# Kernel tuning notes

Measured on AMD Instinct MI355X. Metric: run time of the kernel, lower is better.

## Reference

```python
import jax, jax.numpy as jnp
import numpy as np

N = 50000
E = 800000
F_IN = 256
HID = 64
HEADS = 4
CLASSES = 8
NEG_SLOPE = 0.2  # PyG GATConv default


def setup_inputs() -> dict:
    key = jax.random.key(0)
    ks = jax.random.split(key, 10)
    x = jax.random.normal(ks[0], (N, F_IN), jnp.float32)
    edge_index = jax.random.randint(ks[1], (2, E), 0, N, dtype=jnp.int32)
    # layer 1: feature -> hidden, heads=4, concat
    W1 = jax.random.normal(ks[2], (F_IN, HEADS * HID), jnp.float32) / np.sqrt(F_IN).astype(np.float32)
    att1_src = jax.random.normal(ks[3], (HEADS, HID), jnp.float32) / np.sqrt(HID).astype(np.float32)
    att1_dst = jax.random.normal(ks[4], (HEADS, HID), jnp.float32) / np.sqrt(HID).astype(np.float32)
    b1 = jnp.zeros((HEADS * HID,), jnp.float32)
    # layer 2: hidden*heads -> classes, heads=1
    W2 = jax.random.normal(ks[5], (HEADS * HID, CLASSES), jnp.float32) / np.sqrt(HEADS * HID).astype(np.float32)
    att2_src = jax.random.normal(ks[6], (1, CLASSES), jnp.float32) / np.sqrt(CLASSES).astype(np.float32)
    att2_dst = jax.random.normal(ks[7], (1, CLASSES), jnp.float32) / np.sqrt(CLASSES).astype(np.float32)
    b2 = jnp.zeros((CLASSES,), jnp.float32)
    return {"x": x, "edge_index": edge_index, "W1": W1, "att1_src": att1_src,
            "att1_dst": att1_dst, "b1": b1, "W2": W2, "att2_src": att2_src,
            "att2_dst": att2_dst, "b2": b2}


def _gat_conv(x, W, a_src, a_dst, b, src, dst, heads, ch, n):
    # h: [N, H, C] per-head projected features
    h = (x @ W).reshape(n, heads, ch)
    alpha_src = jnp.einsum('nhc,hc->nh', h, a_src)  # [N, H]
    alpha_dst = jnp.einsum('nhc,hc->nh', h, a_dst)  # [N, H]
    # per-edge attention logits (gather along edges)
    e = jax.nn.leaky_relu(alpha_src[src] + alpha_dst[dst], NEG_SLOPE)  # [E, H]
    # segment softmax over edges sharing a destination node
    e_max = jax.ops.segment_max(e, dst, num_segments=n)  # [N, H]
    ex = jnp.exp(e - e_max[dst])
    denom = jax.ops.segment_sum(ex, dst, num_segments=n)  # [N, H]
    alpha = ex / denom[dst]  # self-loops guarantee denom > 0
    # weighted scatter-sum of source messages
    out = jax.ops.segment_sum(alpha[..., None] * h[src], dst, num_segments=n)  # [N, H, C]
    return out.reshape(n, heads * ch) + b


def reference(x, edge_index, W1, att1_src, att1_dst, b1, W2, att2_src, att2_dst, b2):
    n = x.shape[0]
    # PyG GATConv adds self-loops by default
    loop = jnp.arange(n, dtype=edge_index.dtype)
    src = jnp.concatenate([edge_index[0], loop])
    dst = jnp.concatenate([edge_index[1], loop])
    h = _gat_conv(x, W1, att1_src, att1_dst, b1, src, dst, HEADS, HID, n)
    h = jax.nn.relu(h)
    # dropout is identity in eval mode (training=self.training)
    out = _gat_conv(h, W2, att2_src, att2_dst, b2, src, dst, 1, CLASSES, n)
    return jax.nn.log_softmax(out, axis=1)
```

## Files before the change

kernel.cpp:

```cpp
#include <hip/hip_runtime.h>
#include <math.h>

#define NNODES 50000
#define NEDGES 800000
#define ETOT   850000
#define SLOPE  0.2f
#define BSLOTS 96
#define CPAD   16
#define NTILE  782
#define BBLK   518

typedef unsigned short ushort_t;
typedef unsigned int   uint_t;
typedef __attribute__((ext_vector_type(8))) __bf16 bf16x8;
typedef __attribute__((ext_vector_type(4))) float  floatx4;

__device__ __forceinline__ float leaky(float v) { return fmaxf(v, SLOPE * v); }

__device__ __forceinline__ ushort_t f2bf(float f) {
    uint_t u = __float_as_uint(f);
    uint_t r = (u + 0x7fffu + ((u >> 16) & 1u)) >> 16;
    return (ushort_t)r;
}
__device__ __forceinline__ float lof(uint_t u) { return __uint_as_float(u << 16); }
__device__ __forceinline__ float hif(uint_t u) { return __uint_as_float(u & 0xffff0000u); }

__device__ __forceinline__ float hsel(float4 v, int h) {
    float t0 = (h & 1) ? v.y : v.x;
    float t1 = (h & 1) ? v.w : v.z;
    return (h & 2) ? t1 : t0;
}

__device__ __forceinline__ int esrc(const int* ei, int e) { return e < NEDGES ? ei[e]          : e - NEDGES; }
__device__ __forceinline__ int edst(const int* ei, int e) { return e < NEDGES ? ei[NEDGES + e] : e - NEDGES; }

__global__ void prep_k(const float* __restrict__ W1, ushort_t* __restrict__ W1c,
                       const float* __restrict__ b1, const float* __restrict__ W2,
                       float* __restrict__ b1p, float* __restrict__ W2p,
                       int* __restrict__ cnt) {
    int bid = blockIdx.x, tid = threadIdx.x;
    int gtid = bid * 256 + tid;
    if (bid < 256) {
        int k = gtid >> 8, n = gtid & 255;
        W1c[(k >> 5) * 8192 + n * 32 + (k & 31)] = f2bf(W1[gtid]);
    } else if (bid == 256) {
        int chp = tid;
        int q = chp & 63, cc = q >> 2, t = q & 3;
        int ch = (chp & 192) | (t * 16 + cc);
        b1p[chp] = b1[ch];
        #pragma unroll
        for (int j = 0; j < 8; ++j) W2p[chp * 8 + j] = W2[ch * 8 + j];
    }
    for (int i = gtid; i < NNODES * CPAD; i += 257 * 256) cnt[i] = 0;
}

__global__ __launch_bounds__(256) void gb_k(const float* __restrict__ X,
                                            const ushort_t* __restrict__ W1c,
                                            const float* __restrict__ att_s,
                                            const float* __restrict__ att_d,
                                            ushort_t* __restrict__ h1b,
                                            float* __restrict__ as1,
                                            float* __restrict__ ad1,
                                            const int* __restrict__ ei,
                                            int* __restrict__ cnt,
                                            int* __restrict__ bkt) {
    __shared__ ushort_t Als[64 * 40];
    __shared__ ushort_t Bls[256 * 40];
    int tid = threadIdx.x;

    if (blockIdx.x >= NTILE) {
        for (int e = (blockIdx.x - NTILE) * 256 + tid; e < ETOT; e += BBLK * 256) {
            int d = edst(ei, e), s = esrc(ei, e);
            int pos = atomicAdd(&cnt[d * CPAD], 1);
            if (pos < BSLOTS) bkt[d * BSLOTS + pos] = s;
        }
        return;
    }

    int row0 = blockIdx.x * 64;
    int wv = tid >> 6, lane = tid & 63, c15 = lane & 15, quad = lane >> 4;
    floatx4 acc[4][4] = {};

    for (int kc = 0; kc < 8; ++kc) {
        __syncthreads();
        {
            int r = tid >> 3, c4 = tid & 7;
            #pragma unroll
            for (int p = 0; p < 2; ++p) {
                int rr = r + p * 32;
                int row = row0 + rr;
                float4 v = make_float4(0.f, 0.f, 0.f, 0.f);
                if (row < NNODES) v = *(const float4*)&X[(size_t)row * 256 + kc * 32 + c4 * 4];
                uint2 pk;
                pk.x = (uint_t)f2bf(v.x) | ((uint_t)f2bf(v.y) << 16);
                pk.y = (uint_t)f2bf(v.z) | ((uint_t)f2bf(v.w) << 16);
                *(uint2*)&Als[rr * 40 + c4 * 4] = pk;
            }
        }
        {
            const uint4* srcp = (const uint4*)(W1c + kc * 8192);
            #pragma unroll
            for (int c = 0; c < 4; ++c) {
                int el = tid + c * 256;
                uint4 v = srcp[el];
                int n = el >> 2, kk8 = (el & 3) * 8;
                *(uint4*)&Bls[n * 40 + kk8] = v;
            }
        }
        __syncthreads();
        uint4 af[4], bfr[4];
        #pragma unroll
        for (int t = 0; t < 4; ++t)
            af[t] = *(const uint4*)&Als[(t * 16 + c15) * 40 + quad * 8];
        #pragma unroll
        for (int t = 0; t < 4; ++t)
            bfr[t] = *(const uint4*)&Bls[(wv * 64 + t * 16 + c15) * 40 + quad * 8];
        #pragma unroll
        for (int tm = 0; tm < 4; ++tm)
            #pragma unroll
            for (int tn = 0; tn < 4; ++tn)
                acc[tm][tn] = __builtin_amdgcn_mfma_f32_16x16x32_bf16(
                    __builtin_bit_cast(bf16x8, af[tm]),
                    __builtin_bit_cast(bf16x8, bfr[tn]),
                    acc[tm][tn], 0, 0, 0);
    }

    float asv[4], adv[4];
    #pragma unroll
    for (int tn = 0; tn < 4; ++tn) {
        asv[tn] = att_s[wv * 64 + tn * 16 + c15];
        adv[tn] = att_d[wv * 64 + tn * 16 + c15];
    }
    float ps[4][4], pd[4][4];
    #pragma unroll
    for (int tm = 0; tm < 4; ++tm)
        #pragma unroll
        for (int r = 0; r < 4; ++r) {
            float vs = 0.f, vd = 0.f;
            #pragma unroll
            for (int tn = 0; tn < 4; ++tn) {
                float a = acc[tm][tn][r];
                vs += a * asv[tn]; vd += a * adv[tn];
            }
            ps[tm][r] = vs; pd[tm][r] = vd;
        }
    #pragma unroll
    for (int tm = 0; tm < 4; ++tm) {
        #pragma unroll
        for (int r = 0; r < 4; ++r) {
            int row = row0 + tm * 16 + quad * 4 + r;
            if (row < NNODES) {
                uint2 pk;
                pk.x = (uint_t)f2bf(acc[tm][0][r]) | ((uint_t)f2bf(acc[tm][1][r]) << 16);
                pk.y = (uint_t)f2bf(acc[tm][2][r]) | ((uint_t)f2bf(acc[tm][3][r]) << 16);
                *(uint2*)&h1b[(size_t)row * 256 + wv * 64 + c15 * 4] = pk;
            }
        }
    }
    #pragma unroll
    for (int off = 1; off < 16; off <<= 1)
        #pragma unroll
        for (int tm = 0; tm < 4; ++tm)
            #pragma unroll
            for (int r = 0; r < 4; ++r) {
                ps[tm][r] += __shfl_xor(ps[tm][r], off, 64);
                pd[tm][r] += __shfl_xor(pd[tm][r], off, 64);
            }
    if (c15 == 0) {
        #pragma unroll
        for (int tm = 0; tm < 4; ++tm)
            #pragma unroll
            for (int r = 0; r < 4; ++r) {
                int row = row0 + tm * 16 + quad * 4 + r;
                if (row < NNODES) {
                    as1[row * 4 + wv] = ps[tm][r];
                    ad1[row * 4 + wv] = pd[tm][r];
                }
            }
    }
}

__global__ __launch_bounds__(256) void f1_k(const int* __restrict__ cnt,
                                            const int* __restrict__ bkt,
                                            const float* __restrict__ as1,
                                            const float* __restrict__ ad1,
                                            const ushort_t* __restrict__ h1b,
                                            const float* __restrict__ b1p,
                                            const float* __restrict__ W2p,
                                            const float* __restrict__ a2sw,
                                            const float* __restrict__ a2dw,
                                            float* __restrict__ h2,
                                            float* __restrict__ a2s,
                                            float* __restrict__ a2d) {
    int wv = threadIdx.x >> 6;
    int lane = threadIdx.x & 63;
    int half = lane >> 5, l32 = lane & 31;
    int node = blockIdx.x * 8 + wv * 2 + half;
    int h = l32 >> 3;
    int deg = min(cnt[node * CPAD], BSLOTS);
    const int* bp = bkt + (size_t)node * BSLOTS;
    float4 advec = *(const float4*)&ad1[(size_t)node * 4];
    __shared__ float wls[4][2][32][4];

    float acc[8] = {};
    float dn0, dn1, dn2, dn3;
    if (deg <= 32) {
        bool act = l32 < deg;
        int s_reg = node;
        if (act) s_reg = bp[l32];
        float4 av = *(const float4*)&as1[(size_t)s_reg * 4];
        float e0 = act ? __expf(leaky(av.x + advec.x)) : 0.f;
        float e1 = act ? __expf(leaky(av.y + advec.y)) : 0.f;
        float e2 = act ? __expf(leaky(av.z + advec.z)) : 0.f;
        float e3 = act ? __expf(leaky(av.w + advec.w)) : 0.f;
        *(float4*)&wls[wv][half][l32][0] = make_float4(e0, e1, e2, e3);
        dn0 = e0; dn1 = e1; dn2 = e2; dn3 = e3;
        #pragma unroll
        for (int off = 16; off; off >>= 1) {
            dn0 += __shfl_xor(dn0, off, 64);
            dn1 += __shfl_xor(dn1, off, 64);
            dn2 += __shfl_xor(dn2, off, 64);
            dn3 += __shfl_xor(dn3, off, 64);
        }
        int nb = (deg + 7) & ~7;
        int sbase = half << 5;
        for (int base = 0; base < nb; base += 8) {
            #pragma unroll
            for (int u = 0; u < 8; ++u) {
                int e = base + u;
                int se = __shfl(s_reg, sbase + e, 64);
                float w = wls[wv][half][e][h];
                uint4 v = *(const uint4*)&h1b[(size_t)se * 256 + l32 * 8];
                acc[0] += w * lof(v.x); acc[1] += w * hif(v.x);
                acc[2] += w * lof(v.y); acc[3] += w * hif(v.y);
                acc[4] += w * lof(v.z); acc[5] += w * hif(v.z);
                acc[6] += w * lof(v.w); acc[7] += w * hif(v.w);
            }
        }
    } else {
        dn0 = dn1 = dn2 = dn3 = 0.f;
        for (int j = l32; j < deg; j += 32) {
            int s = bp[j];
            float4 av = *(const float4*)&as1[(size_t)s * 4];
            dn0 += __expf(leaky(av.x + advec.x));
            dn1 += __expf(leaky(av.y + advec.y));
            dn2 += __expf(leaky(av.z + advec.z));
            dn3 += __expf(leaky(av.w + advec.w));
        }
        #pragma unroll
        for (int off = 16; off; off >>= 1) {
            dn0 += __shfl_xor(dn0, off, 64);
            dn1 += __shfl_xor(dn1, off, 64);
            dn2 += __shfl_xor(dn2, off, 64);
            dn3 += __shfl_xor(dn3, off, 64);
        }
        float advh = hsel(advec, h);
        int cmax = deg - 1;
        for (int base = 0; base < deg; base += 8) {
            #pragma unroll
            for (int u = 0; u < 8; ++u) {
                int e = base + u;
                int ce = min(e, cmax);
                int se = bp[ce];
                float ash = as1[(size_t)se * 4 + h];
                float w = (e < deg) ? __expf(leaky(ash + advh)) : 0.f;
                uint4 v = *(const uint4*)&h1b[(size_t)se * 256 + l32 * 8];
                acc[0] += w * lof(v.x); acc[1] += w * hif(v.x);
                acc[2] += w * lof(v.y); acc[3] += w * hif(v.y);
                acc[4] += w * lof(v.z); acc[5] += w * hif(v.z);
                acc[6] += w * lof(v.w); acc[7] += w * hif(v.w);
            }
        }
    }
    float rdh = 1.f / hsel(make_float4(dn0, dn1, dn2, dn3), h);
    #pragma unroll
    for (int c = 0; c < 8; ++c) acc[c] *= rdh;

    int k0 = l32 * 8;
    float4 ba = *(const float4*)&b1p[k0];
    float4 bb = *(const float4*)&b1p[k0 + 4];
    float xv[8];
    xv[0] = fmaxf(acc[0] + ba.x, 0.f); xv[1] = fmaxf(acc[1] + ba.y, 0.f);
    xv[2] = fmaxf(acc[2] + ba.z, 0.f); xv[3] = fmaxf(acc[3] + ba.w, 0.f);
    xv[4] = fmaxf(acc[4] + bb.x, 0.f); xv[5] = fmaxf(acc[5] + bb.y, 0.f);
    xv[6] = fmaxf(acc[6] + bb.z, 0.f); xv[7] = fmaxf(acc[7] + bb.w, 0.f);
    float p[8] = {};
    #pragma unroll
    for (int q = 0; q < 8; ++q) {
        const float4* w2p = (const float4*)&W2p[(size_t)(k0 + q) * 8];
        float4 wa = w2p[0], wb = w2p[1];
        p[0] += xv[q] * wa.x; p[1] += xv[q] * wa.y; p[2] += xv[q] * wa.z; p[3] += xv[q] * wa.w;
        p[4] += xv[q] * wb.x; p[5] += xv[q] * wb.y; p[6] += xv[q] * wb.z; p[7] += xv[q] * wb.w;
    }
    #pragma unroll
    for (int off = 16; off; off >>= 1)
        #pragma unroll
        for (int c = 0; c < 8; ++c) p[c] += __shfl_xor(p[c], off, 64);
    if (l32 == 0) {
        *(float4*)&h2[(size_t)node * 8]     = make_float4(p[0], p[1], p[2], p[3]);
        *(float4*)&h2[(size_t)node * 8 + 4] = make_float4(p[4], p[5], p[6], p[7]);
        float vs = 0.f, vd = 0.f;
        #pragma unroll
        for (int c = 0; c < 8; ++c) { vs += p[c] * a2sw[c]; vd += p[c] * a2dw[c]; }
        a2s[node] = vs; a2d[node] = vd;
    }
}

__global__ __launch_bounds__(256) void f2_k(const int* __restrict__ cnt,
                                            const int* __restrict__ bkt,
                                            const float* __restrict__ a2s,
                                            const float* __restrict__ a2d,
                                            const float* __restrict__ h2,
                                            const float* __restrict__ b2,
                                            float* __restrict__ out) {
    int wv = threadIdx.x >> 6;
    int lane = threadIdx.x & 63;
    int half = lane >> 5, l32 = lane & 31;
    int node = blockIdx.x * 8 + wv * 2 + half;
    int deg = min(cnt[node * CPAD], BSLOTS);
    const int* bp = bkt + (size_t)node * BSLOTS;
    float adv = a2d[node];

    float acc_a = 0.f, acc_b = 0.f;
    float den;
    int c = l32 & 7, eg = l32 >> 3;
    if (deg <= 32) {
        bool act = l32 < deg;
        int s_reg = node;
        if (act) s_reg = bp[l32];
        float ex = act ? __expf(leaky(a2s[s_reg] + adv)) : 0.f;
        den = ex;
        #pragma unroll
        for (int off = 16; off; off >>= 1) den += __shfl_xor(den, off, 64);
        int nb = (deg + 7) & ~7;
        int sbase = half << 5;
        for (int base = 0; base < nb; base += 8) {
            int e1 = base + eg, e2 = base + 4 + eg;
            int se1 = __shfl(s_reg, sbase + e1, 64);
            float w1 = __shfl(ex,    sbase + e1, 64);
            int se2 = __shfl(s_reg, sbase + e2, 64);
            float w2 = __shfl(ex,    sbase + e2, 64);
            acc_a += w1 * h2[(size_t)se1 * 8 + c];
            acc_b += w2 * h2[(size_t)se2 * 8 + c];
        }
    } else {
        den = 0.f;
        for (int j = l32; j < deg; j += 32) {
            int s = bp[j];
            den += __expf(leaky(a2s[s] + adv));
        }
        #pragma unroll
        for (int off = 16; off; off >>= 1) den += __shfl_xor(den, off, 64);
        int cmax = deg - 1;
        for (int base = 0; base < deg; base += 4) {
            int e = base + eg, ce = min(e, cmax);
            int se = bp[ce];
            float w = (e < deg) ? __expf(leaky(a2s[se] + adv)) : 0.f;
            acc_a += w * h2[(size_t)se * 8 + c];
        }
    }
    float acc = acc_a + acc_b;
    acc += __shfl_xor(acc, 8, 64);
    acc += __shfl_xor(acc, 16, 64);
    acc /= den;

    float v = acc + b2[c];
    float mx = v;
    #pragma unroll
    for (int off = 1; off < 8; off <<= 1) mx = fmaxf(mx, __shfl_xor(mx, off, 64));
    float ex2 = __expf(v - mx);
    float ss = ex2;
    #pragma unroll
    for (int off = 1; off < 8; off <<= 1) ss += __shfl_xor(ss, off, 64);
    if (l32 < 8) out[(size_t)node * 8 + c] = v - (mx + __logf(ss));
}

extern "C" void kernel_launch(void* const* d_in, const int* in_sizes, int n_in,
                              void* d_out, int out_size, void* d_ws, size_t ws_size,
                              hipStream_t stream) {
    const float* x    = (const float*)d_in[0];
    const int*   ei   = (const int*)  d_in[1];
    const float* W1   = (const float*)d_in[2];
    const float* a1sw = (const float*)d_in[3];
    const float* a1dw = (const float*)d_in[4];
    const float* b1   = (const float*)d_in[5];
    const float* W2   = (const float*)d_in[6];
    const float* a2sw = (const float*)d_in[7];
    const float* a2dw = (const float*)d_in[8];
    const float* b2   = (const float*)d_in[9];
    float* out = (float*)d_out;

    ushort_t* h1b = (ushort_t*)d_ws;
    ushort_t* W1c = h1b + 12800000;
    float* as1  = (float*)(W1c + 65536);
    float* ad1  = as1 + 200000;
    float* h2   = ad1 + 200000;
    float* a2s  = h2  + 400000;
    float* a2d  = a2s + 50000;
    float* b1p  = a2d + 50000;
    float* W2p  = b1p + 256;
    int*   cnt  = (int*)(W2p + 2048);
    int*   bkt  = cnt + NNODES * CPAD;

    prep_k<<<257, 256, 0, stream>>>(W1, W1c, b1, W2, b1p, W2p, cnt);

    gb_k<<<NTILE + BBLK, 256, 0, stream>>>(x, W1c, a1sw, a1dw, h1b, as1, ad1,
                                           ei, cnt, bkt);

    f1_k<<<NNODES / 8, 256, 0, stream>>>(cnt, bkt, as1, ad1, h1b, b1p, W2p,
                                         a2sw, a2dw, h2, a2s, a2d);

    f2_k<<<NNODES / 8, 256, 0, stream>>>(cnt, bkt, a2s, a2d, h2, b2, out);
}
```

Before: 288.1 us.

## Process two nodes per half-wave in f1 with register-prefetched neighbor gathers

The layer-1 aggregation kernel now gives each half-wave two destination nodes instead of one. It issues the gathers of the first 16 bf16 neighbor rows for both nodes into registers before computing the softmax weights. It then alternates consuming one batch while prefetching the next, to keep more independent memory requests in flight and hide gather latency. The grid is halved to match. The cost is much higher register pressure, which can lower occupancy, and a wave now takes the slow path whenever any of its four nodes has more than 32 neighbors.

```diff
diff --git a/kernel.cpp b/kernel.cpp
--- a/kernel.cpp
+++ b/kernel.cpp
@@ -177,6 +177,109 @@
                     ad1[row * 4 + wv] = pd[tm][r];
                 }
             }
+    }
+}
+
+
+#define PREL(SREG, BASE, VV)                                                    \
+    {                                                                           \
+        _Pragma("unroll")                                                       \
+        for (int u = 0; u < 8; ++u) {                                           \
+            int se = __shfl(SREG, sbase + (BASE) + u, 64);                      \
+            VV[u] = *(const uint4*)&h1b[(size_t)se * 256 + l32 * 8];            \
+        }                                                                       \
+    }
+#define CONS(CH, BASE, VV, AC)                                                  \
+    {                                                                           \
+        _Pragma("unroll")                                                       \
+        for (int u = 0; u < 8; ++u) {                                           \
+            float w = wls[wv][half][CH][(BASE) + u][h];                         \
+            uint4 v = VV[u];                                                    \
+            AC[0] += w * lof(v.x); AC[1] += w * hif(v.x);                       \
+            AC[2] += w * lof(v.y); AC[3] += w * hif(v.y);                       \
+            AC[4] += w * lof(v.z); AC[5] += w * hif(v.z);                       \
+            AC[6] += w * lof(v.w); AC[7] += w * hif(v.w);                       \
+        }                                                                       \
+    }
+
+__device__ __forceinline__ float4 slow_chain(int node, int deg, const int* bp,
+                                             float4 advec, int l32, int h,
+                                             const float* __restrict__ as1,
+                                             const ushort_t* __restrict__ h1b,
+                                             float* acc) {
+    float dn0 = 0.f, dn1 = 0.f, dn2 = 0.f, dn3 = 0.f;
+    for (int j = l32; j < deg; j += 32) {
+        int s = bp[j];
+        float4 av = *(const float4*)&as1[(size_t)s * 4];
+        dn0 += __expf(leaky(av.x + advec.x));
+        dn1 += __expf(leaky(av.y + advec.y));
+        dn2 += __expf(leaky(av.z + advec.z));
+        dn3 += __expf(leaky(av.w + advec.w));
+    }
+    #pragma unroll
+    for (int off = 16; off; off >>= 1) {
+        dn0 += __shfl_xor(dn0, off, 64);
+        dn1 += __shfl_xor(dn1, off, 64);
+        dn2 += __shfl_xor(dn2, off, 64);
+        dn3 += __shfl_xor(dn3, off, 64);
+    }
+    float advh = hsel(advec, h);
+    int cmax = deg - 1;
+    for (int base = 0; base < deg; base += 8) {
+        #pragma unroll
+        for (int u = 0; u < 8; ++u) {
+            int e = base + u;
+            int ce = min(e, cmax);
+            int se = bp[ce];
+            float ash = as1[(size_t)se * 4 + h];
+            float w = (e < deg) ? __expf(leaky(ash + advh)) : 0.f;
+            uint4 v = *(const uint4*)&h1b[(size_t)se * 256 + l32 * 8];
+            acc[0] += w * lof(v.x); acc[1] += w * hif(v.x);
+            acc[2] += w * lof(v.y); acc[3] += w * hif(v.y);
+            acc[4] += w * lof(v.z); acc[5] += w * hif(v.z);
+            acc[6] += w * lof(v.w); acc[7] += w * hif(v.w);
+        }
+    }
+    return make_float4(dn0, dn1, dn2, dn3);
+}
+
+__device__ __forceinline__ void epi(float* acc, float rdh, int node, int l32,
+                                    const float* __restrict__ b1p,
+                                    const float* __restrict__ W2p,
+                                    const float* __restrict__ a2sw,
+                                    const float* __restrict__ a2dw,
+                                    float* __restrict__ h2,
+                                    float* __restrict__ a2s,
+                                    float* __restrict__ a2d) {
+    int k0 = l32 * 8;
+    float4 ba = *(const float4*)&b1p[k0];
+    float4 bb = *(const float4*)&b1p[k0 + 4];
+    float xv[8];
+    #pragma unroll
+    for (int c = 0; c < 8; ++c) acc[c] *= rdh;
+    xv[0] = fmaxf(acc[0] + ba.x, 0.f); xv[1] = fmaxf(acc[1] + ba.y, 0.f);
+    xv[2] = fmaxf(acc[2] + ba.z, 0.f); xv[3] = fmaxf(acc[3] + ba.w, 0.f);
+    xv[4] = fmaxf(acc[4] + bb.x, 0.f); xv[5] = fmaxf(acc[5] + bb.y, 0.f);
+    xv[6] = fmaxf(acc[6] + bb.z, 0.f); xv[7] = fmaxf(acc[7] + bb.w, 0.f);
+    float p[8] = {};
+    #pragma unroll
+    for (int q = 0; q < 8; ++q) {
+        const float4* w2p = (const float4*)&W2p[(size_t)(k0 + q) * 8];
+        float4 wa2 = w2p[0], wb2 = w2p[1];
+        p[0] += xv[q] * wa2.x; p[1] += xv[q] * wa2.y; p[2] += xv[q] * wa2.z; p[3] += xv[q] * wa2.w;
+        p[4] += xv[q] * wb2.x; p[5] += xv[q] * wb2.y; p[6] += xv[q] * wb2.z; p[7] += xv[q] * wb2.w;
+    }
+    #pragma unroll
+    for (int off = 16; off; off >>= 1)
+        #pragma unroll
+        for (int c = 0; c < 8; ++c) p[c] += __shfl_xor(p[c], off, 64);
+    if (l32 == 0) {
+        *(float4*)&h2[(size_t)node * 8]     = make_float4(p[0], p[1], p[2], p[3]);
+        *(float4*)&h2[(size_t)node * 8 + 4] = make_float4(p[4], p[5], p[6], p[7]);
+        float vs = 0.f, vd = 0.f;
+        #pragma unroll
+        for (int c = 0; c < 8; ++c) { vs += p[c] * a2sw[c]; vd += p[c] * a2dw[c]; }
+        a2s[node] = vs; a2d[node] = vd;
     }
 }
 
@@ -195,115 +298,83 @@
     int wv = threadIdx.x >> 6;
     int lane = threadIdx.x & 63;
     int half = lane >> 5, l32 = lane & 31;
-    int node = blockIdx.x * 8 + wv * 2 + half;
+    int base = blockIdx.x * 16 + wv * 4;
+    int nodeA = base + half;
+    int nodeB = base + 2 + half;
     int h = l32 >> 3;
-    int deg = min(cnt[node * CPAD], BSLOTS);
-    const int* bp = bkt + (size_t)node * BSLOTS;
-    float4 advec = *(const float4*)&ad1[(size_t)node * 4];
-    __shared__ float wls[4][2][32][4];
-
-    float acc[8] = {};
-    float dn0, dn1, dn2, dn3;
-    if (deg <= 32) {
-        bool act = l32 < deg;
-        int s_reg = node;
-        if (act) s_reg = bp[l32];
-        float4 av = *(const float4*)&as1[(size_t)s_reg * 4];
-        float e0 = act ? __expf(leaky(av.x + advec.x)) : 0.f;
-        float e1 = act ? __expf(leaky(av.y + advec.y)) : 0.f;
-        float e2 = act ? __expf(leaky(av.z + advec.z)) : 0.f;
-        float e3 = act ? __expf(leaky(av.w + advec.w)) : 0.f;
-        *(float4*)&wls[wv][half][l32][0] = make_float4(e0, e1, e2, e3);
-        dn0 = e0; dn1 = e1; dn2 = e2; dn3 = e3;
+    int sbase = half << 5;
+    __shared__ float wls[4][2][2][32][4];
+
+    int degA = min(cnt[nodeA * CPAD], BSLOTS);
+    int degB = min(cnt[nodeB * CPAD], BSLOTS);
+    const int* bpA = bkt + (size_t)nodeA * BSLOTS;
+    const int* bpB = bkt + (size_t)nodeB * BSLOTS;
+    float4 advA = *(const float4*)&ad1[(size_t)nodeA * 4];
+    float4 advB = *(const float4*)&ad1[(size_t)nodeB * 4];
+
+    int dmA = max(degA, __shfl_xor(degA, 32, 64));
+    int dmB = max(degB, __shfl_xor(degB, 32, 64));
+
+    float accA[8] = {}, accB[8] = {};
+    float rdhA, rdhB;
+
+    if (max(dmA, dmB) <= 32) {
+        bool actA = l32 < degA, actB = l32 < degB;
+        int sA = actA ? bpA[l32] : nodeA;
+        int sB = actB ? bpB[l32] : nodeB;
+        float4 avA = *(const float4*)&as1[(size_t)sA * 4];
+        float4 avB = *(const float4*)&as1[(size_t)sB * 4];
+
+        uint4 vaA[8], vbA[8], vaB[8], vbB[8];
+        PREL(sA, 0, vaA); PREL(sB, 0, vaB);
+        PREL(sA, 8, vbA); PREL(sB, 8, vbB);
+
+        float eA0 = actA ? __expf(leaky(avA.x + advA.x)) : 0.f;
+        float eA1 = actA ? __expf(leaky(avA.y + advA.y)) : 0.f;
+        float eA2 = actA ? __expf(leaky(avA.z + advA.z)) : 0.f;
+        float eA3 = actA ? __expf(leaky(avA.w + advA.w)) : 0.f;
+        float eB0 = actB ? __expf(leaky(avB.x + advB.x)) : 0.f;
+        float eB1 = actB ? __expf(leaky(avB.y + advB.y)) : 0.f;
+        float eB2 = actB ? __expf(leaky(avB.z + advB.z)) : 0.f;
+        float eB3 = actB ? __expf(leaky(avB.w + advB.w)) : 0.f;
+        *(float4*)&wls[wv][half][0][l32][0] = make_float4(eA0, eA1, eA2, eA3);
+        *(float4*)&wls[wv][half][1][l32][0] = make_float4(eB0, eB1, eB2, eB3);
+        float dA0 = eA0, dA1 = eA1, dA2 = eA2, dA3 = eA3;
+        float dB0 = eB0, dB1 = eB1, dB2 = eB2, dB3 = eB3;
         #pragma unroll
         for (int off = 16; off; off >>= 1) {
-            dn0 += __shfl_xor(dn0, off, 64);
-            dn1 += __shfl_xor(dn1, off, 64);
-            dn2 += __shfl_xor(dn2, off, 64);
-            dn3 += __shfl_xor(dn3, off, 64);
-        }
-        int nb = (deg + 7) & ~7;
-        int sbase = half << 5;
-        for (int base = 0; base < nb; base += 8) {
-            #pragma unroll
-            for (int u = 0; u < 8; ++u) {
-                int e = base + u;
-                int se = __shfl(s_reg, sbase + e, 64);
-                float w = wls[wv][half][e][h];
-                uint4 v = *(const uint4*)&h1b[(size_t)se * 256 + l32 * 8];
-                acc[0] += w * lof(v.x); acc[1] += w * hif(v.x);
-                acc[2] += w * lof(v.y); acc[3] += w * hif(v.y);
-                acc[4] += w * lof(v.z); acc[5] += w * hif(v.z);
-                acc[6] += w * lof(v.w); acc[7] += w * hif(v.w);
-            }
-        }
+            dA0 += __shfl_xor(dA0, off, 64); dA1 += __shfl_xor(dA1, off, 64);
+            dA2 += __shfl_xor(dA2, off, 64); dA3 += __shfl_xor(dA3, off, 64);
+            dB0 += __shfl_xor(dB0, off, 64); dB1 += __shfl_xor(dB1, off, 64);
+            dB2 += __shfl_xor(dB2, off, 64); dB3 += __shfl_xor(dB3, off, 64);
+        }
+        rdhA = 1.f / hsel(make_float4(dA0, dA1, dA2, dA3), h);
+        rdhB = 1.f / hsel(make_float4(dB0, dB1, dB2, dB3), h);
+
+        int nbA = (dmA + 7) >> 3;
+        int nbB = (dmB + 7) >> 3;
+
+        CONS(0, 0, vaA, accA);
+        if (nbA > 2) PREL(sA, 16, vaA);
+        CONS(1, 0, vaB, accB);
+        if (nbB > 2) PREL(sB, 16, vaB);
+        CONS(0, 8, vbA, accA);
+        if (nbA > 3) PREL(sA, 24, vbA);
+        CONS(1, 8, vbB, accB);
+        if (nbB > 3) PREL(sB, 24, vbB);
+        if (nbA > 2) CONS(0, 16, vaA, accA);
+        if (nbB > 2) CONS(1, 16, vaB, accB);
+        if (nbA > 3) CONS(0, 24, vbA, accA);
+        if (nbB > 3) CONS(1, 24, vbB, accB);
     } else {
-        dn0 = dn1 = dn2 = dn3 = 0.f;
-        for (int j = l32; j < deg; j += 32) {
-            int s = bp[j];
-            float4 av = *(const float4*)&as1[(size_t)s * 4];
-            dn0 += __expf(leaky(av.x + advec.x));
-            dn1 += __expf(leaky(av.y + advec.y));
-            dn2 += __expf(leaky(av.z + advec.z));
-            dn3 += __expf(leaky(av.w + advec.w));
-        }
-        #pragma unroll
-        for (int off = 16; off; off >>= 1) {
-            dn0 += __shfl_xor(dn0, off, 64);
-            dn1 += __shfl_xor(dn1, off, 64);
-            dn2 += __shfl_xor(dn2, off, 64);
-            dn3 += __shfl_xor(dn3, off, 64);
-        }
-        float advh = hsel(advec, h);
-        int cmax = deg - 1;
-        for (int base = 0; base < deg; base += 8) {
-            #pragma unroll
-            for (int u = 0; u < 8; ++u) {
-                int e = base + u;
-                int ce = min(e, cmax);
-                int se = bp[ce];
-                float ash = as1[(size_t)se * 4 + h];
-                float w = (e < deg) ? __expf(leaky(ash + advh)) : 0.f;
-                uint4 v = *(const uint4*)&h1b[(size_t)se * 256 + l32 * 8];
-                acc[0] += w * lof(v.x); acc[1] += w * hif(v.x);
-                acc[2] += w * lof(v.y); acc[3] += w * hif(v.y);
-                acc[4] += w * lof(v.z); acc[5] += w * hif(v.z);
-                acc[6] += w * lof(v.w); acc[7] += w * hif(v.w);
-            }
-        }
-    }
-    float rdh = 1.f / hsel(make_float4(dn0, dn1, dn2, dn3), h);
-    #pragma unroll
-    for (int c = 0; c < 8; ++c) acc[c] *= rdh;
-
-    int k0 = l32 * 8;
-    float4 ba = *(const float4*)&b1p[k0];
-    float4 bb = *(const float4*)&b1p[k0 + 4];
-    float xv[8];
-    xv[0] = fmaxf(acc[0] + ba.x, 0.f); xv[1] = fmaxf(acc[1] + ba.y, 0.f);
-    xv[2] = fmaxf(acc[2] + ba.z, 0.f); xv[3] = fmaxf(acc[3] + ba.w, 0.f);
-    xv[4] = fmaxf(acc[4] + bb.x, 0.f); xv[5] = fmaxf(acc[5] + bb.y, 0.f);
-    xv[6] = fmaxf(acc[6] + bb.z, 0.f); xv[7] = fmaxf(acc[7] + bb.w, 0.f);
-    float p[8] = {};
-    #pragma unroll
-    for (int q = 0; q < 8; ++q) {
-        const float4* w2p = (const float4*)&W2p[(size_t)(k0 + q) * 8];
-        float4 wa = w2p[0], wb = w2p[1];
-        p[0] += xv[q] * wa.x; p[1] += xv[q] * wa.y; p[2] += xv[q] * wa.z; p[3] += xv[q] * wa.w;
-        p[4] += xv[q] * wb.x; p[5] += xv[q] * wb.y; p[6] += xv[q] * wb.z; p[7] += xv[q] * wb.w;
-    }
-    #pragma unroll
-    for (int off = 16; off; off >>= 1)
-        #pragma unroll
-        for (int c = 0; c < 8; ++c) p[c] += __shfl_xor(p[c], off, 64);
-    if (l32 == 0) {
-        *(float4*)&h2[(size_t)node * 8]     = make_float4(p[0], p[1], p[2], p[3]);
-        *(float4*)&h2[(size_t)node * 8 + 4] = make_float4(p[4], p[5], p[6], p[7]);
-        float vs = 0.f, vd = 0.f;
-        #pragma unroll
-        for (int c = 0; c < 8; ++c) { vs += p[c] * a2sw[c]; vd += p[c] * a2dw[c]; }
-        a2s[node] = vs; a2d[node] = vd;
-    }
+        float4 dA = slow_chain(nodeA, degA, bpA, advA, l32, h, as1, h1b, accA);
+        float4 dB = slow_chain(nodeB, degB, bpB, advB, l32, h, as1, h1b, accB);
+        rdhA = 1.f / hsel(dA, h);
+        rdhB = 1.f / hsel(dB, h);
+    }
+
+    epi(accA, rdhA, nodeA, l32, b1p, W2p, a2sw, a2dw, h2, a2s, a2d);
+    epi(accB, rdhB, nodeB, l32, b1p, W2p, a2sw, a2dw, h2, a2s, a2d);
 }
 
 __global__ __launch_bounds__(256) void f2_k(const int* __restrict__ cnt,
@@ -407,8 +478,8 @@
     gb_k<<<NTILE + BBLK, 256, 0, stream>>>(x, W1c, a1sw, a1dw, h1b, as1, ad1,
                                            ei, cnt, bkt);
 
-    f1_k<<<NNODES / 8, 256, 0, stream>>>(cnt, bkt, as1, ad1, h1b, b1p, W2p,
-                                         a2sw, a2dw, h2, a2s, a2d);
+    f1_k<<<NNODES / 16, 256, 0, stream>>>(cnt, bkt, as1, ad1, h1b, b1p, W2p,
+                                          a2sw, a2dw, h2, a2s, a2d);
 
     f2_k<<<NNODES / 8, 256, 0, stream>>>(cnt, bkt, a2s, a2d, h2, b2, out);
 }
```

After: 299.6 us. 1.04x slower.
